# Optimization experiments

Measured on AMD Instinct MI355X. Metric: run time of the kernel, lower is better.

The kernel has to match this reference:

```python
import jax, jax.numpy as jnp
import numpy as np

EPS = 1e-12  # matches torch.nn.functional.normalize default eps


def _normalize(v):
    # L2 normalize along last dim, clamping the norm like torch F.normalize
    n = jnp.linalg.norm(v, axis=-1, keepdims=True)
    return v / jnp.maximum(n, EPS)


def setup_inputs() -> dict:
    key = jax.random.key(0)
    k1, k2 = jax.random.split(key)
    B, K, D, H, W = 64, 5, 1024, 32, 32
    cue = jax.random.normal(k1, (B, K, D), dtype=jnp.float32)
    patches = jax.random.normal(k2, (B, H, W, D), dtype=jnp.float32)
    return {"cue": cue, "patches": patches}


def reference(cue, patches):
    b, k, d = cue.shape
    _, h, w, _ = patches.shape
    cue_n = _normalize(cue)
    patches_n = _normalize(patches)
    flat = patches_n.reshape(b, h * w, d)
    # cosine similarity between each cue and every patch
    sims = jnp.einsum('bkd,bnd->bkn', cue_n, flat)  # (b, k, h*w)
    idx = jnp.argmax(sims, axis=-1)                 # (b, k)
    y = idx // w + 1                                # +1 for pad offset
    x = idx % w + 1
    # zero-pad spatial dims by 1 on each side
    pad = jnp.pad(patches, ((0, 0), (1, 1), (1, 1), (0, 0)))
    offs = jnp.arange(-1, 2)
    yy = y[:, :, None, None] + offs[None, None, :, None]  # (b, k, 3, 1)
    xx = x[:, :, None, None] + offs[None, None, None, :]  # (b, k, 1, 3)
    bidx = jnp.arange(b)[:, None, None, None]
    gathered = pad[bidx, yy, xx, :]                 # (b, k, 3, 3, d)
    roi = gathered.mean(axis=(2, 3))                # (b, k, d)
    return roi
```

## Files before the change

### kernel.cpp

```cpp
#include <hip/hip_runtime.h>
#include <math.h>

#define B 64
#define K 5
#define D 1024
#define H 32
#define W 32
#define N (H * W)

__device__ __forceinline__ float wave_sum(float v) {
#pragma unroll
    for (int off = 32; off > 0; off >>= 1) v += __shfl_down(v, off, 64);
    return v;
}

__global__ __launch_bounds__(256) void normalize_cue(const float* __restrict__ cue,
                                                     float* __restrict__ cue_n) {
    const int row = blockIdx.x;
    const int tid = threadIdx.x;
    const float4* src = (const float4*)(cue + (size_t)row * D);
    float4 p = src[tid];
    float ss = p.x * p.x + p.y * p.y + p.z * p.z + p.w * p.w;
    ss = wave_sum(ss);
    __shared__ float smem[4];
    __shared__ float s_inv;
    const int lane = tid & 63, wid = tid >> 6;
    if (lane == 0) smem[wid] = ss;
    __syncthreads();
    if (tid == 0) {
        float t = smem[0] + smem[1] + smem[2] + smem[3];
        s_inv = 1.0f / fmaxf(sqrtf(t), 1e-12f);
    }
    __syncthreads();
    const float inv = s_inv;
    float4 o = make_float4(p.x * inv, p.y * inv, p.z * inv, p.w * inv);
    ((float4*)(cue_n + (size_t)row * D))[tid] = o;
}

__global__ __launch_bounds__(256) void sims_kernel(const float* __restrict__ patches,
                                                   const float* __restrict__ cue_n,
                                                   float* __restrict__ sims) {
    const int bn = blockIdx.x;
    const int b = bn >> 10;
    const int n = bn & (N - 1);
    const int tid = threadIdx.x;

    const float4* prow = (const float4*)(patches + (size_t)bn * D);
    float4 p = prow[tid];

    float acc[1 + K];
    acc[0] = p.x * p.x + p.y * p.y + p.z * p.z + p.w * p.w;
    const float4* crow = (const float4*)(cue_n + (size_t)b * K * D);
#pragma unroll
    for (int k = 0; k < K; ++k) {
        float4 c = crow[(size_t)k * (D / 4) + tid];
        acc[1 + k] = p.x * c.x + p.y * c.y + p.z * c.z + p.w * c.w;
    }

    const int lane = tid & 63, wid = tid >> 6;
    __shared__ float smem[4][1 + K];
#pragma unroll
    for (int j = 0; j < 1 + K; ++j) {
        float v = wave_sum(acc[j]);
        if (lane == 0) smem[wid][j] = v;
    }
    __syncthreads();
    if (tid == 0) {
        float t[1 + K];
#pragma unroll
        for (int j = 0; j < 1 + K; ++j)
            t[j] = smem[0][j] + smem[1][j] + smem[2][j] + smem[3][j];
        const float inv = 1.0f / fmaxf(sqrtf(t[0]), 1e-12f);
#pragma unroll
        for (int k = 0; k < K; ++k)
            sims[((size_t)b * K + k) * N + n] = t[1 + k] * inv;
    }
}

__global__ __launch_bounds__(256) void argmax_gather(const float* __restrict__ sims,
                                                     const float* __restrict__ patches,
                                                     float* __restrict__ out) {
    const int row = blockIdx.x;
    const int b = row / K;
    const int tid = threadIdx.x;

    const float* srow = sims + (size_t)row * N;
    float best = -INFINITY;
    int bidx = 0;
#pragma unroll
    for (int j = 0; j < 4; ++j) {
        const int d = tid * 4 + j;
        const float v = srow[d];
        if (v > best) { best = v; bidx = d; }
    }
#pragma unroll
    for (int off = 32; off > 0; off >>= 1) {
        const float ov = __shfl_down(best, off, 64);
        const int oi = __shfl_down(bidx, off, 64);
        if (ov > best || (ov == best && oi < bidx)) { best = ov; bidx = oi; }
    }
    __shared__ float sv[4];
    __shared__ int si[4];
    __shared__ int s_final;
    const int lane = tid & 63, wid = tid >> 6;
    if (lane == 0) { sv[wid] = best; si[wid] = bidx; }
    __syncthreads();
    if (tid == 0) {
        float bv = sv[0];
        int bi = si[0];
        for (int w2 = 1; w2 < 4; ++w2) {
            if (sv[w2] > bv || (sv[w2] == bv && si[w2] < bi)) { bv = sv[w2]; bi = si[w2]; }
        }
        s_final = bi;
    }
    __syncthreads();

    const int idx = s_final;
    const int y0 = idx >> 5;
    const int x0 = idx & 31;

    float4 acc = make_float4(0.f, 0.f, 0.f, 0.f);
#pragma unroll
    for (int dy = -1; dy <= 1; ++dy) {
        const int yy = y0 + dy;
        if (yy < 0 || yy >= H) continue;
#pragma unroll
        for (int dx = -1; dx <= 1; ++dx) {
            const int xx = x0 + dx;
            if (xx < 0 || xx >= W) continue;
            const float4* nrow =
                (const float4*)(patches + (((size_t)b * H + yy) * W + xx) * D);
            float4 p = nrow[tid];
            acc.x += p.x; acc.y += p.y; acc.z += p.z; acc.w += p.w;
        }
    }
    const float inv9 = 1.0f / 9.0f;
    float4 o = make_float4(acc.x * inv9, acc.y * inv9, acc.z * inv9, acc.w * inv9);
    ((float4*)(out + (size_t)row * D))[tid] = o;
}

extern "C" void kernel_launch(void* const* d_in, const int* in_sizes, int n_in,
                              void* d_out, int out_size, void* d_ws, size_t ws_size,
                              hipStream_t stream) {
    const float* cue = (const float*)d_in[0];
    const float* patches = (const float*)d_in[1];
    float* out = (float*)d_out;

    float* cue_n = (float*)d_ws;
    float* sims = cue_n + (size_t)B * K * D;

    normalize_cue<<<B * K, 256, 0, stream>>>(cue, cue_n);
    sims_kernel<<<B * N, 256, 0, stream>>>(patches, cue_n, sims);
    argmax_gather<<<B * K, 256, 0, stream>>>(sims, patches, out);
}
```

Measured before the change: 385.6 us.

## Process two patches per wave in sims kernel to reuse cue loads

Each wave now computes norms and cue dot products for two patch rows, and each block covers eight patches instead of one. Cue vectors loaded once are reused for both patches, which halves cue traffic per patch, and the cross-wave shared-memory reduction and __syncthreads are replaced by pure wave reductions. This adds register pressure and more serial reduction work per wave. The kernel is dominated by streaming the 256MB of patches, so the main cost may not change much.

```diff
diff --git a/kernel.cpp b/kernel.cpp
--- a/kernel.cpp
+++ b/kernel.cpp
@@ -12,6 +12,10 @@
 #pragma unroll
     for (int off = 32; off > 0; off >>= 1) v += __shfl_down(v, off, 64);
     return v;
+}
+
+__device__ __forceinline__ float dot4(float4 a, float4 b) {
+    return a.x * b.x + a.y * b.y + a.z * b.z + a.w * b.w;
 }
 
 __global__ __launch_bounds__(256) void normalize_cue(const float* __restrict__ cue,
@@ -40,40 +44,52 @@
 __global__ __launch_bounds__(256) void sims_kernel(const float* __restrict__ patches,
                                                    const float* __restrict__ cue_n,
                                                    float* __restrict__ sims) {
-    const int bn = blockIdx.x;
-    const int b = bn >> 10;
-    const int n = bn & (N - 1);
-    const int tid = threadIdx.x;
+    const int wave = threadIdx.x >> 6;
+    const int lane = threadIdx.x & 63;
+    const int bn0 = blockIdx.x * 8 + wave * 2;
+    const int b = bn0 >> 10;
+    const int n0 = bn0 & (N - 1);
 
-    const float4* prow = (const float4*)(patches + (size_t)bn * D);
-    float4 p = prow[tid];
+    const float4* p0 = (const float4*)(patches + (size_t)bn0 * D);
+    const float4* p1 = (const float4*)(patches + (size_t)(bn0 + 1) * D);
+    const float4* crow = (const float4*)(cue_n + (size_t)b * K * D);
 
-    float acc[1 + K];
-    acc[0] = p.x * p.x + p.y * p.y + p.z * p.z + p.w * p.w;
-    const float4* crow = (const float4*)(cue_n + (size_t)b * K * D);
+    float na = 0.f, nb = 0.f;
+    float da[K], db[K];
+#pragma unroll
+    for (int k = 0; k < K; ++k) { da[k] = 0.f; db[k] = 0.f; }
+
+#pragma unroll
+    for (int j = 0; j < 4; ++j) {
+        const int idx = j * 64 + lane;
+        float4 pa = p0[idx];
+        float4 pb = p1[idx];
+        na += dot4(pa, pa);
+        nb += dot4(pb, pb);
+#pragma unroll
+        for (int k = 0; k < K; ++k) {
+            float4 c = crow[(size_t)k * (D / 4) + idx];
+            da[k] += dot4(pa, c);
+            db[k] += dot4(pb, c);
+        }
+    }
+
+    na = wave_sum(na);
+    nb = wave_sum(nb);
 #pragma unroll
     for (int k = 0; k < K; ++k) {
-        float4 c = crow[(size_t)k * (D / 4) + tid];
-        acc[1 + k] = p.x * c.x + p.y * c.y + p.z * c.z + p.w * c.w;
+        da[k] = wave_sum(da[k]);
+        db[k] = wave_sum(db[k]);
     }
 
-    const int lane = tid & 63, wid = tid >> 6;
-    __shared__ float smem[4][1 + K];
+    if (lane == 0) {
+        const float ia = 1.0f / fmaxf(sqrtf(na), 1e-12f);
+        const float ib = 1.0f / fmaxf(sqrtf(nb), 1e-12f);
 #pragma unroll
-    for (int j = 0; j < 1 + K; ++j) {
-        float v = wave_sum(acc[j]);
-        if (lane == 0) smem[wid][j] = v;
-    }
-    __syncthreads();
-    if (tid == 0) {
-        float t[1 + K];
-#pragma unroll
-        for (int j = 0; j < 1 + K; ++j)
-            t[j] = smem[0][j] + smem[1][j] + smem[2][j] + smem[3][j];
-        const float inv = 1.0f / fmaxf(sqrtf(t[0]), 1e-12f);
-#pragma unroll
-        for (int k = 0; k < K; ++k)
-            sims[((size_t)b * K + k) * N + n] = t[1 + k] * inv;
+        for (int k = 0; k < K; ++k) {
+            sims[((size_t)b * K + k) * N + n0] = da[k] * ia;
+            sims[((size_t)b * K + k) * N + n0 + 1] = db[k] * ib;
+        }
     }
 }
 
@@ -150,6 +166,6 @@
     float* sims = cue_n + (size_t)B * K * D;
 
     normalize_cue<<<B * K, 256, 0, stream>>>(cue, cue_n);
-    sims_kernel<<<B * N, 256, 0, stream>>>(patches, cue_n, sims);
+    sims_kernel<<<(B * N) / 8, 256, 0, stream>>>(patches, cue_n, sims);
     argmax_gather<<<B * K, 256, 0, stream>>>(sims, patches, out);
 }
```

Result: faster. 364.9 us (-5.4%).
